# Performance work log

Hardware: AMD Instinct MI355X
Metric: run time of the kernel (lower is better)

Reference implementation:

```python
import jax, jax.numpy as jnp
import numpy as np

H = 1024

def setup_inputs() -> dict:
    key = jax.random.key(0)
    ks = jax.random.split(key, 9)
    s = 1.0 / np.sqrt(H)
    x = jax.random.normal(ks[0], (4, 2048, H), dtype=jnp.float32)
    Wq = jax.random.uniform(ks[1], (H, H), jnp.float32, -s, s)
    bq = jax.random.uniform(ks[2], (H,), jnp.float32, -s, s)
    Wk = jax.random.uniform(ks[3], (H, H), jnp.float32, -s, s)
    bk = jax.random.uniform(ks[4], (H,), jnp.float32, -s, s)
    Wv = jax.random.uniform(ks[5], (H, H), jnp.float32, -s, s)
    bv = jax.random.uniform(ks[6], (H,), jnp.float32, -s, s)
    Wo = jax.random.uniform(ks[7], (H, H), jnp.float32, -s, s)
    bo = jax.random.uniform(ks[8], (H,), jnp.float32, -s, s)
    return {"x": x, "Wq": Wq, "bq": bq, "Wk": Wk, "bk": bk,
            "Wv": Wv, "bv": bv, "Wo": Wo, "bo": bo}

def reference(x, Wq, bq, Wk, bk, Wv, bv, Wo, bo):
    # Linear uses y = x @ W.T + b (torch convention: W is [out, in])
    q = jnp.einsum('bsd,ed->bse', x, Wq) + bq
    k = jnp.einsum('bsd,ed->bse', x, Wk) + bk
    v = jnp.einsum('bsd,ed->bse', x, Wv) + bv
    scale = q.shape[-1] ** 0.5
    attn = jnp.einsum('bqe,bke->bqk', q, k) / scale  # [B,S,S]
    attn = jax.nn.softmax(attn, axis=-1)
    out = jnp.einsum('bqk,bke->bqe', attn, v)
    return jnp.einsum('bse,oe->bso', out, Wo) + bo
```

## Files before the change

### kernel.cpp

```cpp
#include <hip/hip_runtime.h>

typedef short  short4v __attribute__((ext_vector_type(4)));
typedef short  short8v __attribute__((ext_vector_type(8)));
typedef __bf16 bf16x8  __attribute__((ext_vector_type(8)));
typedef float  f32x4   __attribute__((ext_vector_type(4)));
typedef float  float4v __attribute__((ext_vector_type(4)));

__device__ __forceinline__ short f2bf(float f) {
  unsigned u = __builtin_bit_cast(unsigned, f);
  u += 0x7fffu + ((u >> 16) & 1u);
  return (short)(u >> 16);
}
__device__ __forceinline__ float bf2f(short h) {
  unsigned u = ((unsigned)(unsigned short)h) << 16;
  return __builtin_bit_cast(float, u);
}
__device__ __forceinline__ bf16x8 ld8(const short* p) {
  return __builtin_bit_cast(bf16x8, *reinterpret_cast<const short8v*>(p));
}

__global__ __launch_bounds__(256) void k_cvt(const float* __restrict__ in,
                                             short* __restrict__ out, int n4) {
  int i = blockIdx.x * 256 + threadIdx.x;
  if (i >= n4) return;
  float4v v = *reinterpret_cast<const float4v*>(in + (long)i * 4);
  short4v o;
  o[0] = f2bf(v[0]); o[1] = f2bf(v[1]); o[2] = f2bf(v[2]); o[3] = f2bf(v[3]);
  *reinterpret_cast<short4v*>(out + (long)i * 4) = o;
}

__global__ __launch_bounds__(256) void k_cvtT(const float* __restrict__ i0,
    const float* __restrict__ i1, const float* __restrict__ i2,
    const float* __restrict__ i3, short* __restrict__ o0, short* __restrict__ o1,
    short* __restrict__ o2, short* __restrict__ o3) {
  const int z = blockIdx.z;
  const float* in = z == 0 ? i0 : z == 1 ? i1 : z == 2 ? i2 : i3;
  short* out = z == 0 ? o0 : z == 1 ? o1 : z == 2 ? o2 : o3;
  __shared__ float tile[16][17];
  const int lx = threadIdx.x & 15, ly = threadIdx.x >> 4;
  const int bx = blockIdx.x << 4, by = blockIdx.y << 4;
  float v = in[(long)(by + ly) * 1024 + bx + lx];
  if (z == 3) {
    out[(long)(by + ly) * 1024 + bx + lx] = f2bf(v);
    return;
  }
  tile[ly][lx] = v;
  __syncthreads();
  out[(long)(bx + ly) * 1024 + by + lx] = f2bf(tile[lx][ly]);
}

__global__ __launch_bounds__(256) void k_matvec(const float* __restrict__ W,
    const float* __restrict__ v, float* __restrict__ o) {
  const int row = blockIdx.x * 4 + (threadIdx.x >> 6), lane = threadIdx.x & 63;
  float s = 0.f;
#pragma unroll
  for (int j = 0; j < 16; ++j)
    s += W[(long)row * 1024 + j * 64 + lane] * v[j * 64 + lane];
#pragma unroll
  for (int off = 32; off; off >>= 1) s += __shfl_xor(s, off);
  if (lane == 0) o[row] = s;
}

__global__ __launch_bounds__(256) void k_rowdot(const short* __restrict__ X,
    const float* __restrict__ v, float* __restrict__ o) {
  const int row = blockIdx.x * 4 + (threadIdx.x >> 6), lane = threadIdx.x & 63;
  const short* xr = X + (long)row * 1024 + lane * 16;
  short8v a0 = *reinterpret_cast<const short8v*>(xr);
  short8v a1 = *reinterpret_cast<const short8v*>(xr + 8);
  float s = 0.f;
#pragma unroll
  for (int j = 0; j < 8; ++j) s += bf2f(a0[j]) * v[lane * 16 + j];
#pragma unroll
  for (int j = 0; j < 8; ++j) s += bf2f(a1[j]) * v[lane * 16 + 8 + j];
#pragma unroll
  for (int off = 32; off; off >>= 1) s += __shfl_xor(s, off);
  if (lane == 0) o[row] = s;
}

template <int MODE>
__global__ __launch_bounds__(256, 3) void k_gemm(
    const short* __restrict__ A, const short* __restrict__ B,
    const float* __restrict__ b0p, float* __restrict__ b1p,
    void* __restrict__ C0,
    int K, int lda, int ldb, long sA, long sB, long sC, int ldC) {
  int bx, by, bz;
  {
    const int gx = gridDim.x, gy = gridDim.y;
    const int n = gx * gy * gridDim.z;
    int f = blockIdx.x + gx * (blockIdx.y + gy * blockIdx.z);
    int s = (n & 7) ? f : ((f & 7) * (n >> 3) + (f >> 3));
    bx = s % gx; int rem = s / gx; by = rem % gy; bz = rem / gy;
  }
  __shared__ __align__(16) short lsA[128 * 64];
  __shared__ __align__(16) short lsB[128 * 64];
  __shared__ float invL[128];
  const int tid = threadIdx.x;
  const int lane = tid & 63, wid = tid >> 6;
  const int wr = wid >> 1, wc = wid & 1;
  const int fr = lane & 15, fq = lane >> 4;
  const int bm = bx * 128, bn = by * 128;
  const short* Ab = A + (long)bz * sA;
  const short* Bb = B + (long)bz * sB;

  if constexpr (MODE == 4) {
    if (tid < 128) {
      const float* pr = b1p + ((long)bz * 2048 + bm + tid) * 32;
      float s = 0.f;
#pragma unroll
      for (int j = 0; j < 32; ++j) s += pr[j];
      invL[tid] = 1.0f / s;
    }
  }

  f32x4 acc[4][4] = {};

  for (int kt = 0; kt < K; kt += 64) {
    __syncthreads();
#pragma unroll
    for (int c = 0; c < 4; ++c) {
      const int idx = c * 256 + tid;
      const int row = idx >> 3, colh = (idx & 7) << 3;
      const short* ga = Ab + (long)(bm + row) * lda + kt + colh;
      const short* gb = Bb + (long)(bn + row) * ldb + kt + colh;
      __builtin_amdgcn_global_load_lds(
          (const __attribute__((address_space(1))) void*)ga,
          (__attribute__((address_space(3))) void*)&lsA[idx * 8], 16, 0, 0);
      __builtin_amdgcn_global_load_lds(
          (const __attribute__((address_space(1))) void*)gb,
          (__attribute__((address_space(3))) void*)&lsB[idx * 8], 16, 0, 0);
    }
    __syncthreads();
#pragma unroll
    for (int ks = 0; ks < 64; ks += 32) {
      bf16x8 a[4], b[4];
#pragma unroll
      for (int m = 0; m < 4; ++m)
        a[m] = ld8(&lsA[(wr * 64 + m * 16 + fr) * 64 + ks + fq * 8]);
#pragma unroll
      for (int n = 0; n < 4; ++n)
        b[n] = ld8(&lsB[(wc * 64 + n * 16 + fr) * 64 + ks + fq * 8]);
#pragma unroll
      for (int m = 0; m < 4; ++m)
#pragma unroll
        for (int n = 0; n < 4; ++n)
          acc[m][n] = __builtin_amdgcn_mfma_f32_16x16x32_bf16(a[m], b[n], acc[m][n], 0, 0, 0);
    }
  }

  if constexpr (MODE == 3) {
    short* O = (short*)C0 + (long)bz * sC;
    float wv[4];
#pragma unroll
    for (int n = 0; n < 4; ++n)
      wv[n] = b0p[(long)bz * 2048 + bn + wc * 64 + n * 16 + fr];
#pragma unroll
    for (int m = 0; m < 4; ++m) {
#pragma unroll
      for (int i = 0; i < 4; ++i) {
        const int row = bm + wr * 64 + m * 16 + fq * 4 + i;
        float rs = 0.f;
#pragma unroll
        for (int n = 0; n < 4; ++n) {
          float e = __expf((acc[m][n][i] + wv[n]) * 0.03125f);
          O[(long)row * ldC + bn + wc * 64 + n * 16 + fr] = f2bf(e);
          rs += e;
        }
        rs += __shfl_xor(rs, 1); rs += __shfl_xor(rs, 2);
        rs += __shfl_xor(rs, 4); rs += __shfl_xor(rs, 8);
        if (fr == 0)
          b1p[((long)bz * 2048 + row) * 32 + (by << 1) + wc] = rs;
      }
    }
  } else {
#pragma unroll
    for (int n = 0; n < 4; ++n) {
      const int coll = wc * 64 + n * 16 + fr;
#pragma unroll
      for (int m = 0; m < 4; ++m) {
        const int rl0 = wr * 64 + m * 16 + fq * 4;
#pragma unroll
        for (int i = 0; i < 4; ++i) {
          const float vacc = acc[m][n][i];
          const long row = bm + rl0 + i, col = bn + coll;
          if constexpr (MODE == 0) {
            ((short*)C0)[((long)bz * sC) + row * ldC + col] = f2bf(vacc);
          } else if constexpr (MODE == 5) {
            ((short*)C0)[row * ldC + col] = f2bf(vacc + b0p[row]);
          } else {
            float* O = (float*)C0 + (long)bz * sC;
            O[row * ldC + col] = vacc * invL[rl0 + i] + b0p[col];
          }
        }
      }
    }
  }
}

extern "C" void kernel_launch(void* const* d_in, const int* in_sizes, int n_in,
                              void* d_out, int out_size, void* d_ws, size_t ws_size,
                              hipStream_t stream) {
  const float* x  = (const float*)d_in[0];
  const float* Wq = (const float*)d_in[1];
  const float* bq = (const float*)d_in[2];
  const float* Wk = (const float*)d_in[3];
  const float* Wv = (const float*)d_in[5];
  const float* bv = (const float*)d_in[6];
  const float* Wo = (const float*)d_in[7];
  const float* bo = (const float*)d_in[8];

  char* ws = (char*)d_ws;
  short* xb   = (short*)ws; ws += 8192L * 1024 * 2;
  short* wkT  = (short*)ws; ws += 1024L * 1024 * 2;
  short* wob  = (short*)ws; ws += 1024L * 1024 * 2;
  short* wqT  = (short*)ws; ws += 1024L * 1024 * 2;
  short* wvT  = (short*)ws; ws += 1024L * 1024 * 2;
  short* mt   = (short*)ws; ws += 1024L * 1024 * 2;
  short* wv2  = (short*)ws; ws += 1024L * 1024 * 2;
  short* T    = (short*)ws; ws += 8192L * 1024 * 2;
  short* vTp  = (short*)ws; ws += 1024L * 8192 * 2;
  short* Sc   = (short*)ws; ws += 4L * 2048 * 2048 * 2;
  float* psum = (float*)ws; ws += 4L * 2048 * 32 * 4;
  float* w8   = (float*)ws; ws += 8192L * 4;
  float* bvec = (float*)ws; ws += 1024L * 4;
  float* bvp  = (float*)ws; ws += 1024L * 4;

  dim3 b256(256);
  k_cvt<<<8192, b256, 0, stream>>>(x, xb, 2097152);
  k_cvtT<<<dim3(64, 64, 4), b256, 0, stream>>>(
      Wk, Wq, Wv, Wo, wkT, wqT, wvT, wob);
  k_rowdot<<<256, b256, 0, stream>>>(wkT, bq, bvec);
  k_matvec<<<256, b256, 0, stream>>>(Wo, bv, bvp);
  k_rowdot<<<2048, b256, 0, stream>>>(xb, bvec, w8);

  k_gemm<0><<<dim3(8, 8, 2), b256, 0, stream>>>(
      wkT, wqT, nullptr, nullptr, mt,
      1024, 1024, 1024, 1024L * 1024, 1024L * 1024, 1024L * 1024, 1024);
  k_gemm<0><<<dim3(64, 8, 1), b256, 0, stream>>>(
      xb, mt, nullptr, nullptr, T, 1024, 1024, 1024, 0, 0, 0, 1024);
  k_gemm<5><<<dim3(8, 64, 1), b256, 0, stream>>>(
      wv2, xb, bvp, nullptr, vTp, 1024, 1024, 1024, 0, 0, 0, 8192);
  k_gemm<3><<<dim3(16, 16, 4), b256, 0, stream>>>(
      T, xb, w8, psum, Sc,
      1024, 1024, 1024, 2048L * 1024, 2048L * 1024, 2048L * 2048, 2048);
  k_gemm<4><<<dim3(16, 8, 4), b256, 0, stream>>>(
      Sc, vTp, bo, psum, (float*)d_out,
      2048, 2048, 8192, 2048L * 2048, 2048, 2048L * 1024, 1024);
}
```

Baseline: 218.4 us.

## Merge bias matvec kernels, drop block swizzle, use exp2 in softmax

```diff
diff --git a/kernel.cpp b/kernel.cpp
--- a/kernel.cpp
+++ b/kernel.cpp
@@ -49,16 +49,28 @@
   out[(long)(bx + ly) * 1024 + by + lx] = f2bf(tile[lx][ly]);
 }
 
-__global__ __launch_bounds__(256) void k_matvec(const float* __restrict__ W,
-    const float* __restrict__ v, float* __restrict__ o) {
+__global__ __launch_bounds__(256) void k_vecprep(
+    const short* __restrict__ wkT, const float* __restrict__ bq,
+    const float* __restrict__ Wo, const float* __restrict__ bv,
+    float* __restrict__ bvec, float* __restrict__ bvp) {
   const int row = blockIdx.x * 4 + (threadIdx.x >> 6), lane = threadIdx.x & 63;
   float s = 0.f;
-#pragma unroll
-  for (int j = 0; j < 16; ++j)
-    s += W[(long)row * 1024 + j * 64 + lane] * v[j * 64 + lane];
+  if (blockIdx.z == 0) {
+    const short* xr = wkT + (long)row * 1024 + lane * 16;
+    short8v a0 = *reinterpret_cast<const short8v*>(xr);
+    short8v a1 = *reinterpret_cast<const short8v*>(xr + 8);
+#pragma unroll
+    for (int j = 0; j < 8; ++j) s += bf2f(a0[j]) * bq[lane * 16 + j];
+#pragma unroll
+    for (int j = 0; j < 8; ++j) s += bf2f(a1[j]) * bq[lane * 16 + 8 + j];
+  } else {
+#pragma unroll
+    for (int j = 0; j < 16; ++j)
+      s += Wo[(long)row * 1024 + j * 64 + lane] * bv[j * 64 + lane];
+  }
 #pragma unroll
   for (int off = 32; off; off >>= 1) s += __shfl_xor(s, off);
-  if (lane == 0) o[row] = s;
+  if (lane == 0) (blockIdx.z == 0 ? bvec : bvp)[row] = s;
 }
 
 __global__ __launch_bounds__(256) void k_rowdot(const short* __restrict__ X,
@@ -83,14 +95,6 @@
     const float* __restrict__ b0p, float* __restrict__ b1p,
     void* __restrict__ C0,
     int K, int lda, int ldb, long sA, long sB, long sC, int ldC) {
-  int bx, by, bz;
-  {
-    const int gx = gridDim.x, gy = gridDim.y;
-    const int n = gx * gy * gridDim.z;
-    int f = blockIdx.x + gx * (blockIdx.y + gy * blockIdx.z);
-    int s = (n & 7) ? f : ((f & 7) * (n >> 3) + (f >> 3));
-    bx = s % gx; int rem = s / gx; by = rem % gy; bz = rem / gy;
-  }
   __shared__ __align__(16) short lsA[128 * 64];
   __shared__ __align__(16) short lsB[128 * 64];
   __shared__ float invL[128];
@@ -98,7 +102,8 @@
   const int lane = tid & 63, wid = tid >> 6;
   const int wr = wid >> 1, wc = wid & 1;
   const int fr = lane & 15, fq = lane >> 4;
-  const int bm = bx * 128, bn = by * 128;
+  const int bm = blockIdx.x * 128, bn = blockIdx.y * 128;
+  const int bz = blockIdx.z;
   const short* Ab = A + (long)bz * sA;
   const short* Bb = B + (long)bz * sB;
 
@@ -148,6 +153,7 @@
   }
 
   if constexpr (MODE == 3) {
+    constexpr float c = 0.03125f * 1.44269504f;
     short* O = (short*)C0 + (long)bz * sC;
     float wv[4];
 #pragma unroll
@@ -161,14 +167,14 @@
         float rs = 0.f;
 #pragma unroll
         for (int n = 0; n < 4; ++n) {
-          float e = __expf((acc[m][n][i] + wv[n]) * 0.03125f);
+          float e = exp2f((acc[m][n][i] + wv[n]) * c);
           O[(long)row * ldC + bn + wc * 64 + n * 16 + fr] = f2bf(e);
           rs += e;
         }
         rs += __shfl_xor(rs, 1); rs += __shfl_xor(rs, 2);
         rs += __shfl_xor(rs, 4); rs += __shfl_xor(rs, 8);
         if (fr == 0)
-          b1p[((long)bz * 2048 + row) * 32 + (by << 1) + wc] = rs;
+          b1p[((long)bz * 2048 + row) * 32 + (blockIdx.y << 1) + wc] = rs;
       }
     }
   } else {
@@ -228,8 +234,7 @@
   k_cvt<<<8192, b256, 0, stream>>>(x, xb, 2097152);
   k_cvtT<<<dim3(64, 64, 4), b256, 0, stream>>>(
       Wk, Wq, Wv, Wo, wkT, wqT, wvT, wob);
-  k_rowdot<<<256, b256, 0, stream>>>(wkT, bq, bvec);
-  k_matvec<<<256, b256, 0, stream>>>(Wo, bv, bvp);
+  k_vecprep<<<dim3(256, 1, 2), b256, 0, stream>>>(wkT, bq, Wo, bv, bvec, bvp);
   k_rowdot<<<2048, b256, 0, stream>>>(xb, bvec, w8);
 
   k_gemm<0><<<dim3(8, 8, 2), b256, 0, stream>>>(
```

After: 212.3 us. 1.03x faster.
